# Kernel tuning notes

Hardware: AMD Instinct MI355X
Metric: run time of the kernel (lower is better)

Reference implementation:

```python
import jax, jax.numpy as jnp
import numpy as np


def setup_inputs() -> dict:
    key = jax.random.key(0)
    k1, k2, k3, k4, k5 = jax.random.split(key, 5)
    B, S, DK, D = 64, 2048, 1024, 1024
    hidden_state = jax.random.normal(k1, (B, D), dtype=jnp.float32)
    encoder_outputs = jax.random.normal(k2, (B, S, DK), dtype=jnp.float32)
    # linear1: in = dim_key + dim*num_layers = 2048, out = dim = 1024
    W1 = jax.random.normal(k3, (D, DK + D), dtype=jnp.float32) * (1.0 / np.sqrt(DK + D))
    b1 = jax.random.normal(k4, (D,), dtype=jnp.float32) * 0.01
    W2 = jax.random.normal(k5, (1, D), dtype=jnp.float32) * (1.0 / np.sqrt(D))
    return {"hidden_state": hidden_state, "encoder_outputs": encoder_outputs,
            "W1": W1, "b1": b1, "W2": W2}


def reference(hidden_state, encoder_outputs, W1, b1, W2):
    # torch: cat([enc, h], -1) @ W1.T  ==  enc @ W1e.T + h @ W1h.T
    # (split avoids materializing the [B,S,DK+D] concat; same math)
    DK = encoder_outputs.shape[-1]
    W1e, W1h = W1[:, :DK], W1[:, DK:]
    # pre: [B, S, D]
    pre = (jnp.einsum('bsk,dk->bsd', encoder_outputs, W1e)
           + jnp.einsum('bm,dm->bd', hidden_state, W1h)[:, None, :]
           + b1)
    e = jnp.einsum('bsd,d->bs', jnp.tanh(pre), W2[0])  # scores [B, S]
    alpha = jax.nn.softmax(e, axis=1)
    context = jnp.einsum('bs,bsk->bk', alpha, encoder_outputs)  # [B, DK]
    return context
```

## Files before the change

### kernel.cpp

```cpp
#include <hip/hip_runtime.h>

typedef __attribute__((ext_vector_type(8))) short short8;
typedef __attribute__((ext_vector_type(4))) float floatx4;

#define M_TOT 131072
#define SEQ   2048
#define NB    8

__device__ __forceinline__ unsigned bf16rne(float x) {
  unsigned u = __float_as_uint(x);
  return (u + 0x7FFFu + ((u >> 16) & 1u)) >> 16;
}

#define GLOAD_LDS16(g, l) __builtin_amdgcn_global_load_lds( \
    (const __attribute__((address_space(1))) unsigned int*)(g), \
    (__attribute__((address_space(3))) unsigned int*)(l), 16, 0, 0)

__global__ __launch_bounds__(256) void convert_enc_kernel(
    const float* __restrict__ in, unsigned int* __restrict__ out)
{
  size_t i = ((size_t)blockIdx.x * 256 + threadIdx.x) * 8;
  float4 a = *(const float4*)(in + i);
  float4 b = *(const float4*)(in + i + 4);
  uint4 o;
  o.x = bf16rne(a.x) | (bf16rne(a.y) << 16);
  o.y = bf16rne(a.z) | (bf16rne(a.w) << 16);
  o.z = bf16rne(b.x) | (bf16rne(b.y) << 16);
  o.w = bf16rne(b.z) | (bf16rne(b.w) << 16);
  *(uint4*)(out + i / 2) = o;
}

__global__ __launch_bounds__(128) void convert_w1e_kernel(
    const float* __restrict__ W1, unsigned int* __restrict__ out)
{
  int d = blockIdx.x;
  int k = threadIdx.x * 8;
  const float* p = W1 + (size_t)d * 2048 + k;
  float4 a = *(const float4*)p;
  float4 b = *(const float4*)(p + 4);
  uint4 o;
  o.x = bf16rne(a.x) | (bf16rne(a.y) << 16);
  o.y = bf16rne(a.z) | (bf16rne(a.w) << 16);
  o.z = bf16rne(b.x) | (bf16rne(b.y) << 16);
  o.w = bf16rne(b.z) | (bf16rne(b.w) << 16);
  *(uint4*)(out + ((size_t)d * 1024 + k) / 2) = o;
}

__global__ __launch_bounds__(256) void hvec_kernel(
    const float* __restrict__ hid, const float* __restrict__ W1,
    const float* __restrict__ b1, float* __restrict__ hvec)
{
  int b = blockIdx.x, g = blockIdx.y;
  int w = threadIdx.x >> 6, lane = threadIdx.x & 63;
  const float* hrow = hid + b * 1024;
  for (int i = 0; i < 4; ++i) {
    int d = g * 16 + w * 4 + i;
    const float* wrow = W1 + (size_t)d * 2048 + 1024;
    float sum = 0.f;
#pragma unroll
    for (int c = 0; c < 4; ++c) {
      int m = c * 256 + lane * 4;
      float4 wv = *(const float4*)(wrow + m);
      float4 hv = *(const float4*)(hrow + m);
      sum += wv.x * hv.x + wv.y * hv.y + wv.z * hv.z + wv.w * hv.w;
    }
#pragma unroll
    for (int msk = 1; msk < 64; msk <<= 1) sum += __shfl_xor(sum, msk);
    if (lane == 0) hvec[b * 1024 + d] = sum + b1[d];
  }
}

__global__ __launch_bounds__(512, 2) void gemm256_kernel(
    const unsigned short* __restrict__ A, const unsigned short* __restrict__ B,
    const float* __restrict__ W2, const float* __restrict__ hvec,
    float* __restrict__ epart)
{
  __shared__ __align__(16) unsigned short lds[4][2][8192];

  const int tid = threadIdx.x;
  const int lid = blockIdx.x;
  const int xcd = lid & 7, q = lid >> 3;
  const int mb = xcd * 64 + (q >> 2);
  const int nb = q & 3;
  const int r0 = mb * 256, n0 = nb * 256;
  const int bidx = r0 >> 11;
  const int wid = tid >> 6, lane = tid & 63;
  const int wm = wid >> 2, wn = wid & 3;
  const int lrow = lane & 15, kq = lane >> 4;

  int offA[2], offB[2], dst[2];
#pragma unroll
  for (int j = 0; j < 2; ++j) {
    int c = tid + j * 512;
    int r = c >> 2, s = c & 3;
    offA[j] = (r0 + r) * 1024 + s * 8;
    offB[j] = (n0 + r) * 1024 + s * 8;
    dst[j] = (wid * 64 + j * 512) * 8;
  }

  floatx4 acc[8][4];
#pragma unroll
  for (int i = 0; i < 8; ++i)
#pragma unroll
    for (int j = 0; j < 4; ++j)
      acc[i][j] = (floatx4){0.f, 0.f, 0.f, 0.f};

#define STAGE_J(T, J) do { \
    GLOAD_LDS16(A + (size_t)offA[J] + (T) * 32, &lds[(T) & 3][0][dst[J]]); \
    GLOAD_LDS16(B + (size_t)offB[J] + (T) * 32, &lds[(T) & 3][1][dst[J]]); \
  } while (0)

  STAGE_J(0, 0); STAGE_J(0, 1);
  STAGE_J(1, 0); STAGE_J(1, 1);

  const int aB = wm * 4096 + lrow * 32 + kq * 8;
  const int bB = wn * 2048 + lrow * 32 + kq * 8;

  asm volatile("s_waitcnt vmcnt(4)" ::: "memory");
  __builtin_amdgcn_s_barrier();

  for (int tt = 0; tt < 8; ++tt) {
#pragma unroll
    for (int u = 0; u < 4; ++u) {
      const int t = tt * 4 + u;
      const unsigned short* Ah = lds[u][0];
      const unsigned short* Bh = lds[u][1];

      short8 af[8], bf[4];
#pragma unroll
      for (int mt = 0; mt < 4; ++mt) af[mt] = *(const short8*)&Ah[aB + mt * 512];
#pragma unroll
      for (int nt = 0; nt < 4; ++nt) bf[nt] = *(const short8*)&Bh[bB + nt * 512];
      if (t < 30) STAGE_J(t + 2, 0);
      __builtin_amdgcn_s_barrier();
      asm volatile("s_waitcnt lgkmcnt(0)" ::: "memory");
      __builtin_amdgcn_sched_barrier(0);
      __builtin_amdgcn_s_setprio(1);
#pragma unroll
      for (int mt = 0; mt < 4; ++mt)
#pragma unroll
        for (int nt = 0; nt < 4; ++nt)
          acc[mt][nt] = __builtin_amdgcn_mfma_f32_16x16x32_bf16(
              af[mt], bf[nt], acc[mt][nt], 0, 0, 0);
      __builtin_amdgcn_s_setprio(0);
      __builtin_amdgcn_s_barrier();
#pragma unroll
      for (int mt = 4; mt < 8; ++mt) af[mt] = *(const short8*)&Ah[aB + mt * 512];
      if (t < 30) STAGE_J(t + 2, 1);
      __builtin_amdgcn_s_barrier();
      asm volatile("s_waitcnt lgkmcnt(0)" ::: "memory");
      __builtin_amdgcn_sched_barrier(0);
      __builtin_amdgcn_s_setprio(1);
#pragma unroll
      for (int mt = 4; mt < 8; ++mt)
#pragma unroll
        for (int nt = 0; nt < 4; ++nt)
          acc[mt][nt] = __builtin_amdgcn_mfma_f32_16x16x32_bf16(
              af[mt], bf[nt], acc[mt][nt], 0, 0, 0);
      __builtin_amdgcn_s_setprio(0);
      if (t < 30) { asm volatile("s_waitcnt vmcnt(4)" ::: "memory"); }
      else        { asm volatile("s_waitcnt vmcnt(0)" ::: "memory"); }
      __builtin_amdgcn_s_barrier();
    }
  }
#undef STAGE_J

  __syncthreads();
  float* ep = (float*)&lds[0][0][0];
  float hv[4], w2v[4];
#pragma unroll
  for (int nt = 0; nt < 4; ++nt) {
    int n = n0 + wn * 64 + nt * 16 + lrow;
    hv[nt]  = hvec[bidx * 1024 + n];
    w2v[nt] = W2[n];
  }
#pragma unroll
  for (int mt = 0; mt < 8; ++mt) {
#pragma unroll
    for (int r = 0; r < 4; ++r) {
      float sum = 0.f;
#pragma unroll
      for (int nt = 0; nt < 4; ++nt) {
        float pre = acc[mt][nt][r] + hv[nt];
        float ex = __expf(2.f * pre);
        sum += (1.f - 2.f / (ex + 1.f)) * w2v[nt];
      }
      sum += __shfl_xor(sum, 1);
      sum += __shfl_xor(sum, 2);
      sum += __shfl_xor(sum, 4);
      sum += __shfl_xor(sum, 8);
      if (lrow == 0) ep[wn * 256 + wm * 128 + mt * 16 + kq * 4 + r] = sum;
    }
  }
  __syncthreads();
  if (tid < 256) {
    float s = ep[tid] + ep[256 + tid] + ep[512 + tid] + ep[768 + tid];
    epart[(size_t)nb * M_TOT + r0 + tid] = s;
  }
}

__global__ __launch_bounds__(256) void fused_gemm_kernel(
    const float* __restrict__ enc, const float* __restrict__ W1,
    const float* __restrict__ W2, const float* __restrict__ hvec,
    float* __restrict__ epart)
{
  __shared__ __align__(16) unsigned short Ah[128 * 32];
  __shared__ __align__(16) unsigned short Bh[128 * 32];
  __shared__ float ep[2][128];

  const int tid = threadIdx.x;
  const int nb = blockIdx.x, mb = blockIdx.y;
  const int r0 = mb * 128, n0 = nb * 128;
  const int bidx = r0 >> 11;
  const int w = tid >> 6, lane = tid & 63;
  const int wm = w >> 1, wn = w & 1;
  const int lrow = lane & 15, kq = lane >> 4;

  floatx4 acc[4][4];
#pragma unroll
  for (int i = 0; i < 4; ++i)
#pragma unroll
    for (int j = 0; j < 4; ++j)
      acc[i][j] = (floatx4){0.f, 0.f, 0.f, 0.f};

  const int srow = tid >> 3;
  const int scol = (tid & 7) * 4;
  const float* aptr = enc + (size_t)(r0 + srow) * 1024 + scol;
  const float* bptr = W1  + (size_t)(n0 + srow) * 2048 + scol;

  for (int k0 = 0; k0 < 1024; k0 += 32) {
    float4 av[4], bv[4];
#pragma unroll
    for (int j = 0; j < 4; ++j) {
      av[j] = *(const float4*)(aptr + (size_t)(j * 32) * 1024 + k0);
      bv[j] = *(const float4*)(bptr + (size_t)(j * 32) * 2048 + k0);
    }
    __syncthreads();
#pragma unroll
    for (int j = 0; j < 4; ++j) {
      unsigned ax = __float_as_uint(av[j].x), ay = __float_as_uint(av[j].y);
      unsigned az = __float_as_uint(av[j].z), aw = __float_as_uint(av[j].w);
      unsigned a01 = __builtin_amdgcn_perm(ay, ax, 0x07060302u);
      unsigned a23 = __builtin_amdgcn_perm(aw, az, 0x07060302u);
      *(uint2*)&Ah[(tid + j * 256) * 4] = make_uint2(a01, a23);
      unsigned bx = __float_as_uint(bv[j].x), by = __float_as_uint(bv[j].y);
      unsigned bz = __float_as_uint(bv[j].z), bw = __float_as_uint(bv[j].w);
      unsigned b01 = __builtin_amdgcn_perm(by, bx, 0x07060302u);
      unsigned b23 = __builtin_amdgcn_perm(bw, bz, 0x07060302u);
      *(uint2*)&Bh[(tid + j * 256) * 4] = make_uint2(b01, b23);
    }
    __syncthreads();

    short8 af[4], bfm[4];
#pragma unroll
    for (int t4 = 0; t4 < 4; ++t4) {
      af[t4]  = *(const short8*)&Ah[(wm * 64 + t4 * 16 + lrow) * 32 + kq * 8];
      bfm[t4] = *(const short8*)&Bh[(wn * 64 + t4 * 16 + lrow) * 32 + kq * 8];
    }
#pragma unroll
    for (int mt = 0; mt < 4; ++mt)
#pragma unroll
      for (int nt = 0; nt < 4; ++nt)
        acc[mt][nt] = __builtin_amdgcn_mfma_f32_16x16x32_bf16(
            af[mt], bfm[nt], acc[mt][nt], 0, 0, 0);
  }

  float hv[4], w2v[4];
#pragma unroll
  for (int nt = 0; nt < 4; ++nt) {
    int n = n0 + wn * 64 + nt * 16 + lrow;
    hv[nt]  = hvec[bidx * 1024 + n];
    w2v[nt] = W2[n];
  }
#pragma unroll
  for (int mt = 0; mt < 4; ++mt) {
#pragma unroll
    for (int r = 0; r < 4; ++r) {
      float sum = 0.f;
#pragma unroll
      for (int nt = 0; nt < 4; ++nt) {
        float pre = acc[mt][nt][r] + hv[nt];
        float ex = __expf(2.f * pre);
        sum += (1.f - 2.f / (ex + 1.f)) * w2v[nt];
      }
      sum += __shfl_xor(sum, 1);
      sum += __shfl_xor(sum, 2);
      sum += __shfl_xor(sum, 4);
      sum += __shfl_xor(sum, 8);
      if (lrow == 0) ep[wn][wm * 64 + mt * 16 + kq * 4 + r] = sum;
    }
  }
  __syncthreads();
  if (tid < 128)
    epart[(size_t)nb * M_TOT + r0 + tid] = ep[0][tid] + ep[1][tid];
}

template<int NP>
__global__ __launch_bounds__(256) void softmax_kernel(
    const float* __restrict__ epart, float* __restrict__ alpha)
{
  int b = blockIdx.x, t = threadIdx.x;
  __shared__ float redmax[4], redsum[4];
  float ev[8];
  float lmax = -1e30f;
#pragma unroll
  for (int j = 0; j < 8; ++j) {
    int s = t + j * 256;
    float sum = 0.f;
#pragma unroll
    for (int p = 0; p < NP; ++p) sum += epart[(size_t)p * M_TOT + b * SEQ + s];
    ev[j] = sum;
    lmax = fmaxf(lmax, sum);
  }
#pragma unroll
  for (int msk = 1; msk < 64; msk <<= 1) lmax = fmaxf(lmax, __shfl_xor(lmax, msk));
  if ((t & 63) == 0) redmax[t >> 6] = lmax;
  __syncthreads();
  float bmax = fmaxf(fmaxf(redmax[0], redmax[1]), fmaxf(redmax[2], redmax[3]));
  float lsum = 0.f;
#pragma unroll
  for (int j = 0; j < 8; ++j) { ev[j] = __expf(ev[j] - bmax); lsum += ev[j]; }
#pragma unroll
  for (int msk = 1; msk < 64; msk <<= 1) lsum += __shfl_xor(lsum, msk);
  if ((t & 63) == 0) redsum[t >> 6] = lsum;
  __syncthreads();
  float inv = 1.f / (redsum[0] + redsum[1] + redsum[2] + redsum[3]);
#pragma unroll
  for (int j = 0; j < 8; ++j) alpha[b * SEQ + t + j * 256] = ev[j] * inv;
}

__global__ __launch_bounds__(512) void context_bf16_kernel(
    const unsigned int* __restrict__ encB, const float* __restrict__ alpha,
    float* __restrict__ out)
{
  __shared__ float red[16][128];
  int b = blockIdx.x, kc = blockIdx.y, t = threadIdx.x;
  int kl = (t & 31) * 4;
  int strip = t >> 5;
  const unsigned int* ep = encB +
      (((size_t)b * SEQ + strip * 128) * 1024 + kc * 128 + kl) / 2;
  const float* ap = alpha + b * SEQ + strip * 128;
  float a0 = 0.f, a1 = 0.f, a2 = 0.f, a3 = 0.f;
#pragma unroll 4
  for (int s = 0; s < 128; ++s) {
    float a = ap[s];
    uint2 v = *(const uint2*)(ep + (size_t)s * 512);
    a0 += a * __uint_as_float(v.x << 16);
    a1 += a * __uint_as_float(v.x & 0xFFFF0000u);
    a2 += a * __uint_as_float(v.y << 16);
    a3 += a * __uint_as_float(v.y & 0xFFFF0000u);
  }
  red[strip][kl + 0] = a0;
  red[strip][kl + 1] = a1;
  red[strip][kl + 2] = a2;
  red[strip][kl + 3] = a3;
  __syncthreads();
  if (t < 128) {
    float s = 0.f;
#pragma unroll
    for (int j = 0; j < 16; ++j) s += red[j][t];
    out[b * 1024 + kc * 128 + t] = s;
  }
}

__global__ __launch_bounds__(256) void context_kernel(
    const float* __restrict__ enc, const float* __restrict__ alpha,
    float* __restrict__ out)
{
  int b = blockIdx.y, sq = blockIdx.z, t = threadIdx.x;
  int k4 = t * 4;
  const float* ep = enc + ((size_t)b * SEQ + sq * 128) * 1024 + k4;
  const float* ap = alpha + b * SEQ + sq * 128;
  float ax = 0.f, ay = 0.f, az = 0.f, aw = 0.f;
#pragma unroll 4
  for (int s = 0; s < 128; ++s) {
    float a = ap[s];
    float4 v = *(const float4*)(ep + (size_t)s * 1024);
    ax += a * v.x; ay += a * v.y; az += a * v.z; aw += a * v.w;
  }
  float* o = out + b * 1024 + k4;
  atomicAdd(o + 0, ax);
  atomicAdd(o + 1, ay);
  atomicAdd(o + 2, az);
  atomicAdd(o + 3, aw);
}

extern "C" void kernel_launch(void* const* d_in, const int* in_sizes, int n_in,
                              void* d_out, int out_size, void* d_ws, size_t ws_size,
                              hipStream_t stream) {
  const float* hid = (const float*)d_in[0];
  const float* enc = (const float*)d_in[1];
  const float* W1  = (const float*)d_in[2];
  const float* b1  = (const float*)d_in[3];
  const float* W2  = (const float*)d_in[4];
  float* out = (float*)d_out;

  float* epart = (float*)d_ws;
  float* alpha = epart + (size_t)NB * M_TOT;
  float* hvec  = alpha + M_TOT;
  size_t small_bytes = ((size_t)NB * M_TOT + M_TOT + 64 * 1024) * 4;
  size_t encB_off = ((small_bytes + 255) / 256) * 256;
  size_t need = encB_off + (size_t)M_TOT * 1024 * 2 + (size_t)1024 * 1024 * 2;

  hvec_kernel<<<dim3(64, 64), 256, 0, stream>>>(hid, W1, b1, hvec);

  if (ws_size >= need) {
    unsigned short* encB = (unsigned short*)((char*)d_ws + encB_off);
    unsigned short* W1eB = encB + (size_t)M_TOT * 1024;
    convert_enc_kernel<<<65536, 256, 0, stream>>>(enc, (unsigned int*)encB);
    convert_w1e_kernel<<<1024, 128, 0, stream>>>(W1, (unsigned int*)W1eB);
    gemm256_kernel<<<2048, 512, 0, stream>>>(encB, W1eB, W2, hvec, epart);
    softmax_kernel<4><<<64, 256, 0, stream>>>(epart, alpha);
    context_bf16_kernel<<<dim3(64, 8), 512, 0, stream>>>((unsigned int*)encB, alpha, out);
  } else {
    hipMemsetAsync(d_out, 0, (size_t)out_size * sizeof(float), stream);
    fused_gemm_kernel<<<dim3(NB, 1024), 256, 0, stream>>>(enc, W1, W2, hvec, epart);
    softmax_kernel<8><<<64, 256, 0, stream>>>(epart, alpha);
    context_kernel<<<dim3(1, 64, 16), 256, 0, stream>>>(enc, alpha, out);
  }
}
```

Baseline: 1.091 ms.

## Double-buffer MFMA fragments in registers and cut barriers to one per k-tile

The bf16 GEMM main loop is restructured so the next k-tile's A-low and B fragments are read from LDS into a second register set while the current tile's upper-half MFMAs run. Both global-to-LDS stages for tile t+2 are issued together at the start of each tile. The four barriers and two lgkmcnt(0) waits per tile become a single vmcnt wait plus one barrier. The aim is to hide LDS latency behind matrix math and remove synchronisation stalls, at the cost of extra VGPRs for the ping-pong fragment buffers and reliance on the compiler to schedule the LDS waits.

After: 1.092 ms. No clear change (+0.1%).

```diff
diff --git a/kernel.cpp b/kernel.cpp
--- a/kernel.cpp
+++ b/kernel.cpp
@@ -110,59 +110,60 @@
     GLOAD_LDS16(B + (size_t)offB[J] + (T) * 32, &lds[(T) & 3][1][dst[J]]); \
   } while (0)
 
+  const int aB = wm * 4096 + lrow * 32 + kq * 8;
+  const int bB = wn * 2048 + lrow * 32 + kq * 8;
+
   STAGE_J(0, 0); STAGE_J(0, 1);
   STAGE_J(1, 0); STAGE_J(1, 1);
-
-  const int aB = wm * 4096 + lrow * 32 + kq * 8;
-  const int bB = wn * 2048 + lrow * 32 + kq * 8;
-
   asm volatile("s_waitcnt vmcnt(4)" ::: "memory");
   __builtin_amdgcn_s_barrier();
 
-  for (int tt = 0; tt < 8; ++tt) {
-#pragma unroll
-    for (int u = 0; u < 4; ++u) {
-      const int t = tt * 4 + u;
-      const unsigned short* Ah = lds[u][0];
-      const unsigned short* Bh = lds[u][1];
-
-      short8 af[8], bf[4];
-#pragma unroll
-      for (int mt = 0; mt < 4; ++mt) af[mt] = *(const short8*)&Ah[aB + mt * 512];
-#pragma unroll
-      for (int nt = 0; nt < 4; ++nt) bf[nt] = *(const short8*)&Bh[bB + nt * 512];
-      if (t < 30) STAGE_J(t + 2, 0);
-      __builtin_amdgcn_s_barrier();
-      asm volatile("s_waitcnt lgkmcnt(0)" ::: "memory");
-      __builtin_amdgcn_sched_barrier(0);
-      __builtin_amdgcn_s_setprio(1);
-#pragma unroll
-      for (int mt = 0; mt < 4; ++mt)
-#pragma unroll
-        for (int nt = 0; nt < 4; ++nt)
-          acc[mt][nt] = __builtin_amdgcn_mfma_f32_16x16x32_bf16(
-              af[mt], bf[nt], acc[mt][nt], 0, 0, 0);
-      __builtin_amdgcn_s_setprio(0);
-      __builtin_amdgcn_s_barrier();
-#pragma unroll
-      for (int mt = 4; mt < 8; ++mt) af[mt] = *(const short8*)&Ah[aB + mt * 512];
-      if (t < 30) STAGE_J(t + 2, 1);
-      __builtin_amdgcn_s_barrier();
-      asm volatile("s_waitcnt lgkmcnt(0)" ::: "memory");
-      __builtin_amdgcn_sched_barrier(0);
-      __builtin_amdgcn_s_setprio(1);
-#pragma unroll
-      for (int mt = 4; mt < 8; ++mt)
-#pragma unroll
-        for (int nt = 0; nt < 4; ++nt)
-          acc[mt][nt] = __builtin_amdgcn_mfma_f32_16x16x32_bf16(
-              af[mt], bf[nt], acc[mt][nt], 0, 0, 0);
-      __builtin_amdgcn_s_setprio(0);
-      if (t < 30) { asm volatile("s_waitcnt vmcnt(4)" ::: "memory"); }
-      else        { asm volatile("s_waitcnt vmcnt(0)" ::: "memory"); }
-      __builtin_amdgcn_s_barrier();
-    }
-  }
+  short8 afLoA[4], bfA[4], afLoB[4], bfB[4], afHi[4];
+#pragma unroll
+  for (int mt = 0; mt < 4; ++mt) afLoA[mt] = *(const short8*)&lds[0][0][aB + mt * 512];
+#pragma unroll
+  for (int nt = 0; nt < 4; ++nt) bfA[nt]   = *(const short8*)&lds[0][1][bB + nt * 512];
+
+#define TILE_BODY(T, afLoC, bfC, afLoN, bfN) do { \
+    const unsigned short* Ah = lds[(T) & 3][0]; \
+    _Pragma("unroll") \
+    for (int mt = 0; mt < 4; ++mt) afHi[mt] = *(const short8*)&Ah[aB + (mt + 4) * 512]; \
+    if ((T) < 30) { STAGE_J((T) + 2, 0); STAGE_J((T) + 2, 1); } \
+    __builtin_amdgcn_s_setprio(1); \
+    _Pragma("unroll") \
+    for (int mt = 0; mt < 4; ++mt) \
+      _Pragma("unroll") \
+      for (int nt = 0; nt < 4; ++nt) \
+        acc[mt][nt] = __builtin_amdgcn_mfma_f32_16x16x32_bf16( \
+            afLoC[mt], bfC[nt], acc[mt][nt], 0, 0, 0); \
+    __builtin_amdgcn_s_setprio(0); \
+    if ((T) < 31) { \
+      if ((T) < 30) { asm volatile("s_waitcnt vmcnt(4)" ::: "memory"); } \
+      else          { asm volatile("s_waitcnt vmcnt(0)" ::: "memory"); } \
+      __builtin_amdgcn_s_barrier(); \
+      const unsigned short* An = lds[((T) + 1) & 3][0]; \
+      const unsigned short* Bn = lds[((T) + 1) & 3][1]; \
+      _Pragma("unroll") \
+      for (int mt = 0; mt < 4; ++mt) afLoN[mt] = *(const short8*)&An[aB + mt * 512]; \
+      _Pragma("unroll") \
+      for (int nt = 0; nt < 4; ++nt) bfN[nt]   = *(const short8*)&Bn[bB + nt * 512]; \
+    } \
+    __builtin_amdgcn_s_setprio(1); \
+    _Pragma("unroll") \
+    for (int mt = 0; mt < 4; ++mt) \
+      _Pragma("unroll") \
+      for (int nt = 0; nt < 4; ++nt) \
+        acc[mt + 4][nt] = __builtin_amdgcn_mfma_f32_16x16x32_bf16( \
+            afHi[mt], bfC[nt], acc[mt + 4][nt], 0, 0, 0); \
+    __builtin_amdgcn_s_setprio(0); \
+  } while (0)
+
+  for (int tt = 0; tt < 16; ++tt) {
+    const int t0 = tt * 2;
+    TILE_BODY(t0,     afLoA, bfA, afLoB, bfB);
+    TILE_BODY(t0 + 1, afLoB, bfB, afLoA, bfA);
+  }
+#undef TILE_BODY
 #undef STAGE_J
 
   __syncthreads();
```

## Pre-swizzle bf16 operands into MFMA fragment order and restructure GEMM pipeline

Applied to the files above, without the earlier changes.

The conversion kernels now write encoder and W1e bf16 data in a fragment-major layout that matches the MFMA operand order. The GEMM stages contiguous 16-byte chunks with double-buffered 64-wide K tiles and an 8-phase schedule that interleaves register loads with MFMA groups. The context kernel reads the original fp32 encoder instead of the bf16 copy, which restores full precision there but reads twice the bytes. The intent is to cut LDS bank conflicts and address arithmetic in the GEMM main loop, and to overlap loads with compute more finely.

Measured after the change: 1.156 ms. 1.06x slower.

```diff
diff --git a/kernel.cpp b/kernel.cpp
--- a/kernel.cpp
+++ b/kernel.cpp
@@ -16,26 +16,22 @@
     (const __attribute__((address_space(1))) unsigned int*)(g), \
     (__attribute__((address_space(3))) unsigned int*)(l), 16, 0, 0)
 
-__global__ __launch_bounds__(256) void convert_enc_kernel(
+#define VMW4 asm volatile("s_waitcnt vmcnt(4)" ::: "memory")
+#define VMW2 asm volatile("s_waitcnt vmcnt(2)" ::: "memory")
+#define VMW0 asm volatile("s_waitcnt vmcnt(0)" ::: "memory")
+#define BAR() __builtin_amdgcn_s_barrier()
+#define SP(n) __builtin_amdgcn_s_setprio(n)
+
+__global__ __launch_bounds__(256) void convert_enc_frag_kernel(
     const float* __restrict__ in, unsigned int* __restrict__ out)
 {
-  size_t i = ((size_t)blockIdx.x * 256 + threadIdx.x) * 8;
-  float4 a = *(const float4*)(in + i);
-  float4 b = *(const float4*)(in + i + 4);
-  uint4 o;
-  o.x = bf16rne(a.x) | (bf16rne(a.y) << 16);
-  o.y = bf16rne(a.z) | (bf16rne(a.w) << 16);
-  o.z = bf16rne(b.x) | (bf16rne(b.y) << 16);
-  o.w = bf16rne(b.z) | (bf16rne(b.w) << 16);
-  *(uint4*)(out + i / 2) = o;
-}
-
-__global__ __launch_bounds__(128) void convert_w1e_kernel(
-    const float* __restrict__ W1, unsigned int* __restrict__ out)
-{
-  int d = blockIdx.x;
-  int k = threadIdx.x * 8;
-  const float* p = W1 + (size_t)d * 2048 + k;
+  unsigned C = blockIdx.x * 256 + threadIdx.x;
+  int lane = C & 63, ks = (C >> 6) & 1, mtl = (C >> 7) & 3;
+  int wm = (C >> 9) & 1, h = (C >> 10) & 1, t = (C >> 11) & 15;
+  int mb = C >> 15;
+  int row = mb * 256 + wm * 128 + (h * 4 + mtl) * 16 + (lane & 15);
+  int k0 = t * 64 + ks * 32 + (lane >> 4) * 8;
+  const float* p = in + (size_t)row * 1024 + k0;
   float4 a = *(const float4*)p;
   float4 b = *(const float4*)(p + 4);
   uint4 o;
@@ -43,7 +39,27 @@
   o.y = bf16rne(a.z) | (bf16rne(a.w) << 16);
   o.z = bf16rne(b.x) | (bf16rne(b.y) << 16);
   o.w = bf16rne(b.z) | (bf16rne(b.w) << 16);
-  *(uint4*)(out + ((size_t)d * 1024 + k) / 2) = o;
+  *(uint4*)(out + (size_t)C * 4) = o;
+}
+
+__global__ __launch_bounds__(256) void convert_w1e_frag_kernel(
+    const float* __restrict__ W1, unsigned int* __restrict__ out)
+{
+  unsigned G = blockIdx.x * 256 + threadIdx.x;
+  int lane = G & 63, ks = (G >> 6) & 1, ntl = (G >> 7) & 1;
+  int wn = (G >> 8) & 3, h = (G >> 10) & 1, t = (G >> 11) & 15;
+  int nb = G >> 15;
+  int d = nb * 256 + wn * 64 + (h * 2 + ntl) * 16 + (lane & 15);
+  int k0 = t * 64 + ks * 32 + (lane >> 4) * 8;
+  const float* p = W1 + (size_t)d * 2048 + k0;
+  float4 a = *(const float4*)p;
+  float4 b = *(const float4*)(p + 4);
+  uint4 o;
+  o.x = bf16rne(a.x) | (bf16rne(a.y) << 16);
+  o.y = bf16rne(a.z) | (bf16rne(a.w) << 16);
+  o.z = bf16rne(b.x) | (bf16rne(b.y) << 16);
+  o.w = bf16rne(b.z) | (bf16rne(b.w) << 16);
+  *(uint4*)(out + (size_t)G * 4) = o;
 }
 
 __global__ __launch_bounds__(256) void hvec_kernel(
@@ -70,33 +86,26 @@
   }
 }
 
-__global__ __launch_bounds__(512, 2) void gemm256_kernel(
-    const unsigned short* __restrict__ A, const unsigned short* __restrict__ B,
+__global__ __launch_bounds__(512, 2) void gemm256_8ph_kernel(
+    const unsigned short* __restrict__ encB, const unsigned short* __restrict__ W1eB,
     const float* __restrict__ W2, const float* __restrict__ hvec,
     float* __restrict__ epart)
 {
-  __shared__ __align__(16) unsigned short lds[4][2][8192];
+  __shared__ __align__(16) unsigned short ldsA[2][16384];
+  __shared__ __align__(16) unsigned short ldsB[2][16384];
 
   const int tid = threadIdx.x;
   const int lid = blockIdx.x;
   const int xcd = lid & 7, q = lid >> 3;
   const int mb = xcd * 64 + (q >> 2);
   const int nb = q & 3;
-  const int r0 = mb * 256, n0 = nb * 256;
-  const int bidx = r0 >> 11;
+  const int r0 = mb * 256;
+  const int bidx = mb >> 3;
   const int wid = tid >> 6, lane = tid & 63;
   const int wm = wid >> 2, wn = wid & 3;
-  const int lrow = lane & 15, kq = lane >> 4;
-
-  int offA[2], offB[2], dst[2];
-#pragma unroll
-  for (int j = 0; j < 2; ++j) {
-    int c = tid + j * 512;
-    int r = c >> 2, s = c & 3;
-    offA[j] = (r0 + r) * 1024 + s * 8;
-    offB[j] = (n0 + r) * 1024 + s * 8;
-    dst[j] = (wid * 64 + j * 512) * 8;
-  }
+  const int lrow = lane & 15;
+  const int kq = lane >> 4;
+  const int lane8 = lane * 8;
 
   floatx4 acc[8][4];
 #pragma unroll
@@ -105,72 +114,104 @@
     for (int j = 0; j < 4; ++j)
       acc[i][j] = (floatx4){0.f, 0.f, 0.f, 0.f};
 
-#define STAGE_J(T, J) do { \
-    GLOAD_LDS16(A + (size_t)offA[J] + (T) * 32, &lds[(T) & 3][0][dst[J]]); \
-    GLOAD_LDS16(B + (size_t)offB[J] + (T) * 32, &lds[(T) & 3][1][dst[J]]); \
+#define STAGE_A(T, h, sl) do { \
+    const unsigned short* gp = encB + ((size_t)(mb * 16 + (T)) * 2048 + (h) * 1024 + tid) * 8; \
+    GLOAD_LDS16(gp,        &ldsA[sl][((h) * 1024 + wid * 64) * 8]); \
+    GLOAD_LDS16(gp + 4096, &ldsA[sl][((h) * 1024 + 512 + wid * 64) * 8]); \
   } while (0)
-
-  STAGE_J(0, 0); STAGE_J(0, 1);
-  STAGE_J(1, 0); STAGE_J(1, 1);
-
-  const int aB = wm * 4096 + lrow * 32 + kq * 8;
-  const int bB = wn * 2048 + lrow * 32 + kq * 8;
-
-  asm volatile("s_waitcnt vmcnt(4)" ::: "memory");
-  __builtin_amdgcn_s_barrier();
-
-  for (int tt = 0; tt < 8; ++tt) {
-#pragma unroll
-    for (int u = 0; u < 4; ++u) {
-      const int t = tt * 4 + u;
-      const unsigned short* Ah = lds[u][0];
-      const unsigned short* Bh = lds[u][1];
-
-      short8 af[8], bf[4];
-#pragma unroll
-      for (int mt = 0; mt < 4; ++mt) af[mt] = *(const short8*)&Ah[aB + mt * 512];
-#pragma unroll
-      for (int nt = 0; nt < 4; ++nt) bf[nt] = *(const short8*)&Bh[bB + nt * 512];
-      if (t < 30) STAGE_J(t + 2, 0);
-      __builtin_amdgcn_s_barrier();
-      asm volatile("s_waitcnt lgkmcnt(0)" ::: "memory");
-      __builtin_amdgcn_sched_barrier(0);
-      __builtin_amdgcn_s_setprio(1);
+#define STAGE_B(T, h, sl) do { \
+    const unsigned short* gp = W1eB + ((size_t)(nb * 16 + (T)) * 2048 + (h) * 1024 + tid) * 8; \
+    GLOAD_LDS16(gp,        &ldsB[sl][((h) * 1024 + wid * 64) * 8]); \
+    GLOAD_LDS16(gp + 4096, &ldsB[sl][((h) * 1024 + 512 + wid * 64) * 8]); \
+  } while (0)
+
+  const int aRd = wm * 4096 + lane8;
+  const int bRd = wn * 2048 + lane8;
+
+  short8 af[4][2], b0[2][2], b1[2][2];
+
+  STAGE_A(0, 0, 0); STAGE_B(0, 0, 0); STAGE_B(0, 1, 0); STAGE_A(0, 1, 0);
+  VMW4;
+  BAR();
+#pragma unroll
+  for (int mt = 0; mt < 4; ++mt)
+#pragma unroll
+    for (int ks = 0; ks < 2; ++ks)
+      af[mt][ks] = *(const short8*)&ldsA[0][aRd + mt * 1024 + ks * 512];
+#pragma unroll
+  for (int nt = 0; nt < 2; ++nt)
+#pragma unroll
+    for (int ks = 0; ks < 2; ++ks)
+      b0[nt][ks] = *(const short8*)&ldsB[0][bRd + nt * 1024 + ks * 512];
+
+#define MFMA16(R, C, AF, BF) do { \
+    SP(1); \
+    _Pragma("unroll") for (int mt_ = 0; mt_ < 4; ++mt_) \
+    _Pragma("unroll") for (int nt_ = 0; nt_ < 2; ++nt_) \
+    _Pragma("unroll") for (int ks_ = 0; ks_ < 2; ++ks_) \
+      acc[(R) + mt_][(C) + nt_] = __builtin_amdgcn_mfma_f32_16x16x32_bf16( \
+          AF[mt_][ks_], BF[nt_][ks_], acc[(R) + mt_][(C) + nt_], 0, 0, 0); \
+    SP(0); \
+  } while (0)
+
+  for (int tau = 0; tau < 16; ++tau) {
+    const int s = tau & 1, sn = s ^ 1;
+    const unsigned short* As = ldsA[s];
+    const unsigned short* Bs = ldsB[s];
+    const unsigned short* An = ldsA[sn];
+    const unsigned short* Bn = ldsB[sn];
+    const bool more = (tau < 15);
+
+    if (more) { STAGE_A(tau + 1, 0, sn); VMW4; } else { VMW2; }
+    BAR();
+#pragma unroll
+    for (int nt = 0; nt < 2; ++nt)
+#pragma unroll
+      for (int ks = 0; ks < 2; ++ks)
+        b1[nt][ks] = *(const short8*)&Bs[8192 + bRd + nt * 1024 + ks * 512];
+    MFMA16(0, 0, af, b0);
+
+    if (more) { STAGE_B(tau + 1, 0, sn); VMW4; } else { VMW0; }
+    BAR();
+    MFMA16(0, 2, af, b1);
+
+    if (more) { STAGE_B(tau + 1, 1, sn); VMW4; }
+    BAR();
+#pragma unroll
+    for (int mt = 0; mt < 4; ++mt)
+#pragma unroll
+      for (int ks = 0; ks < 2; ++ks)
+        af[mt][ks] = *(const short8*)&As[8192 + aRd + mt * 1024 + ks * 512];
+    MFMA16(4, 0, af, b0);
+
+    if (more) { STAGE_A(tau + 1, 1, sn); VMW4; }
+    BAR();
+    if (more) {
+#pragma unroll
+      for (int nt = 0; nt < 2; ++nt)
+#pragma unroll
+        for (int ks = 0; ks < 2; ++ks)
+          b0[nt][ks] = *(const short8*)&Bn[bRd + nt * 1024 + ks * 512];
+    }
+    MFMA16(4, 2, af, b1);
+    if (more) {
 #pragma unroll
       for (int mt = 0; mt < 4; ++mt)
 #pragma unroll
-        for (int nt = 0; nt < 4; ++nt)
-          acc[mt][nt] = __builtin_amdgcn_mfma_f32_16x16x32_bf16(
-              af[mt], bf[nt], acc[mt][nt], 0, 0, 0);
-      __builtin_amdgcn_s_setprio(0);
-      __builtin_amdgcn_s_barrier();
-#pragma unroll
-      for (int mt = 4; mt < 8; ++mt) af[mt] = *(const short8*)&Ah[aB + mt * 512];
-      if (t < 30) STAGE_J(t + 2, 1);
-      __builtin_amdgcn_s_barrier();
-      asm volatile("s_waitcnt lgkmcnt(0)" ::: "memory");
-      __builtin_amdgcn_sched_barrier(0);
-      __builtin_amdgcn_s_setprio(1);
-#pragma unroll
-      for (int mt = 4; mt < 8; ++mt)
-#pragma unroll
-        for (int nt = 0; nt < 4; ++nt)
-          acc[mt][nt] = __builtin_amdgcn_mfma_f32_16x16x32_bf16(
-              af[mt], bf[nt], acc[mt][nt], 0, 0, 0);
-      __builtin_amdgcn_s_setprio(0);
-      if (t < 30) { asm volatile("s_waitcnt vmcnt(4)" ::: "memory"); }
-      else        { asm volatile("s_waitcnt vmcnt(0)" ::: "memory"); }
-      __builtin_amdgcn_s_barrier();
-    }
-  }
-#undef STAGE_J
-
-  __syncthreads();
-  float* ep = (float*)&lds[0][0][0];
+        for (int ks = 0; ks < 2; ++ks)
+          af[mt][ks] = *(const short8*)&An[aRd + mt * 1024 + ks * 512];
+    }
+  }
+#undef MFMA16
+#undef STAGE_A
+#undef STAGE_B
+
+  __syncthreads();
+  float* ep = (float*)&ldsA[0][0];
   float hv[4], w2v[4];
 #pragma unroll
   for (int nt = 0; nt < 4; ++nt) {
-    int n = n0 + wn * 64 + nt * 16 + lrow;
+    int n = nb * 256 + wn * 64 + nt * 16 + lrow;
     hv[nt]  = hvec[bidx * 1024 + n];
     w2v[nt] = W2[n];
   }
@@ -194,8 +235,8 @@
   }
   __syncthreads();
   if (tid < 256) {
-    float s = ep[tid] + ep[256 + tid] + ep[512 + tid] + ep[768 + tid];
-    epart[(size_t)nb * M_TOT + r0 + tid] = s;
+    float sv = ep[tid] + ep[256 + tid] + ep[512 + tid] + ep[768 + tid];
+    epart[(size_t)nb * M_TOT + r0 + tid] = sv;
   }
 }
 
@@ -329,26 +370,22 @@
   for (int j = 0; j < 8; ++j) alpha[b * SEQ + t + j * 256] = ev[j] * inv;
 }
 
-__global__ __launch_bounds__(512) void context_bf16_kernel(
-    const unsigned int* __restrict__ encB, const float* __restrict__ alpha,
+__global__ __launch_bounds__(512) void context_f32_kernel(
+    const float* __restrict__ enc, const float* __restrict__ alpha,
     float* __restrict__ out)
 {
   __shared__ float red[16][128];
   int b = blockIdx.x, kc = blockIdx.y, t = threadIdx.x;
   int kl = (t & 31) * 4;
   int strip = t >> 5;
-  const unsigned int* ep = encB +
-      (((size_t)b * SEQ + strip * 128) * 1024 + kc * 128 + kl) / 2;
+  const float* ep = enc + ((size_t)b * SEQ + strip * 128) * 1024 + kc * 128 + kl;
   const float* ap = alpha + b * SEQ + strip * 128;
   float a0 = 0.f, a1 = 0.f, a2 = 0.f, a3 = 0.f;
 #pragma unroll 4
   for (int s = 0; s < 128; ++s) {
     float a = ap[s];
-    uint2 v = *(const uint2*)(ep + (size_t)s * 512);
-    a0 += a * __uint_as_float(v.x << 16);
-    a1 += a * __uint_as_float(v.x & 0xFFFF0000u);
-    a2 += a * __uint_as_float(v.y << 16);
-    a3 += a * __uint_as_float(v.y & 0xFFFF0000u);
+    float4 v = *(const float4*)(ep + (size_t)s * 1024);
+    a0 += a * v.x; a1 += a * v.y; a2 += a * v.z; a3 += a * v.w;
   }
   red[strip][kl + 0] = a0;
   red[strip][kl + 1] = a1;
@@ -407,11 +444,11 @@
   if (ws_size >= need) {
     unsigned short* encB = (unsigned short*)((char*)d_ws + encB_off);
     unsigned short* W1eB = encB + (size_t)M_TOT * 1024;
-    convert_enc_kernel<<<65536, 256, 0, stream>>>(enc, (unsigned int*)encB);
-    convert_w1e_kernel<<<1024, 128, 0, stream>>>(W1, (unsigned int*)W1eB);
-    gemm256_kernel<<<2048, 512, 0, stream>>>(encB, W1eB, W2, hvec, epart);
+    convert_enc_frag_kernel<<<65536, 256, 0, stream>>>(enc, (unsigned int*)encB);
+    convert_w1e_frag_kernel<<<512, 256, 0, stream>>>(W1, (unsigned int*)W1eB);
+    gemm256_8ph_kernel<<<2048, 512, 0, stream>>>(encB, W1eB, W2, hvec, epart);
     softmax_kernel<4><<<64, 256, 0, stream>>>(epart, alpha);
-    context_bf16_kernel<<<dim3(64, 8), 512, 0, stream>>>((unsigned int*)encB, alpha, out);
+    context_f32_kernel<<<dim3(64, 8), 512, 0, stream>>>(enc, alpha, out);
   } else {
     hipMemsetAsync(d_out, 0, (size_t)out_size * sizeof(float), stream);
     fused_gemm_kernel<<<dim3(NB, 1024), 256, 0, stream>>>(enc, W1, W2, hvec, epart);
```
